# Performance work log

Hardware: AMD Instinct MI355X
Metric: run time of the kernel (lower is better)

## Reference

```python
import jax, jax.numpy as jnp
import numpy as np

N_NODES = 100000
IN_CH = 128
HID_CH = 128
N_EDGES = 1600000


def setup_inputs() -> dict:
    key = jax.random.key(0)
    ks = jax.random.split(key, 8)
    x = jax.random.normal(ks[0], (N_NODES, IN_CH), dtype=jnp.float32)
    edge_index = jax.random.randint(ks[1], (2, N_EDGES), 0, N_NODES, dtype=jnp.int64)
    s1 = 1.0 / np.sqrt(IN_CH)
    s2 = 1.0 / np.sqrt(HID_CH)
    # SAGEConv layer 1: lin_l (aggregated neighbors, has bias), lin_r (root)
    Wl1 = jax.random.uniform(ks[2], (IN_CH, HID_CH), jnp.float32, -s1, s1)
    Wr1 = jax.random.uniform(ks[3], (IN_CH, HID_CH), jnp.float32, -s1, s1)
    b1 = jnp.zeros((HID_CH,), jnp.float32)
    # SAGEConv layer 2
    Wl2 = jax.random.uniform(ks[4], (HID_CH, HID_CH), jnp.float32, -s2, s2)
    Wr2 = jax.random.uniform(ks[5], (HID_CH, HID_CH), jnp.float32, -s2, s2)
    b2 = jnp.zeros((HID_CH,), jnp.float32)
    return {"x": x, "edge_index": edge_index,
            "Wl1": Wl1, "Wr1": Wr1, "b1": b1,
            "Wl2": Wl2, "Wr2": Wr2, "b2": b2}


def _sage_conv(x, src, dst, inv_deg, Wl, Wr, b):
    # mean aggregation of source-node features into destination nodes
    agg = jax.ops.segment_sum(x[src], dst, num_segments=N_NODES)  # [N, d]
    mean = agg * inv_deg[:, None]
    # out = lin_l(mean_neighbors) + lin_r(x)
    return mean @ Wl + x @ Wr + b


def reference(x, edge_index, Wl1, Wr1, b1, Wl2, Wr2, b2):
    src = edge_index[0]
    dst = edge_index[1]
    deg = jax.ops.segment_sum(jnp.ones_like(dst, dtype=jnp.float32), dst,
                              num_segments=N_NODES)
    inv_deg = 1.0 / jnp.maximum(deg, 1.0)
    h = jax.nn.relu(_sage_conv(x, src, dst, inv_deg, Wl1, Wr1, b1))
    # F.dropout(p=0.2, training=False) is identity in eval mode
    h = jax.nn.relu(_sage_conv(h, src, dst, inv_deg, Wl2, Wr2, b2))
    return h
```

## Files before the change

### kernel.cpp

```cpp
#include <hip/hip_runtime.h>

#define NN 100000
#define NE 1600000
#define CH 128

#define PART 512
#define NP 196
#define PCAP 8704
#define NB 391
#define SCAP 64
#define SLAB 1536

typedef __attribute__((ext_vector_type(8))) short bf16x8;
typedef __attribute__((ext_vector_type(4))) float f32x4;
typedef unsigned int uint;
typedef unsigned short ushort;

__device__ __forceinline__ ushort f2b(float f) {
    uint u = __builtin_bit_cast(uint, f);
    uint r = (u + 0x7fff + ((u >> 16) & 1)) >> 16;
    return (ushort)r;
}
__device__ __forceinline__ float blo(uint v) { return __builtin_bit_cast(float, v << 16); }
__device__ __forceinline__ float bhi(uint v) { return __builtin_bit_cast(float, v & 0xffff0000u); }

__device__ __forceinline__ void acc8(float* a, uint4 v) {
    a[0] += blo(v.x); a[1] += bhi(v.x);
    a[2] += blo(v.y); a[3] += bhi(v.y);
    a[4] += blo(v.z); a[5] += bhi(v.z);
    a[6] += blo(v.w); a[7] += bhi(v.w);
}


__global__ __launch_bounds__(1024) void k_bin(const int4* __restrict__ src4, const int4* __restrict__ dst4,
                                              uint* __restrict__ pcnt, uint* __restrict__ pairbuf) {
    __shared__ uint slots[NP * SCAP];
    __shared__ uint lcnt[NP];
    __shared__ uint lbase[NP];
    int tid = threadIdx.x;
    if (tid < NP) lcnt[tid] = 0;
    __syncthreads();
    int e4 = blockIdx.x * 1024 + tid;
    if (e4 < NE / 4) {
        int4 d4 = dst4[e4];
        int4 s4 = src4[e4];
        int dd[4] = {d4.x, d4.y, d4.z, d4.w};
        int ss[4] = {s4.x, s4.y, s4.z, s4.w};
        #pragma unroll
        for (int j = 0; j < 4; ++j) {
            int p = dd[j] >> 9;
            uint pair = ((uint)(dd[j] & 511) << 17) | (uint)ss[j];
            uint pos = atomicAdd(&lcnt[p], 1u);
            if (pos < SCAP) slots[p * SCAP + pos] = pair;
        }
    }
    __syncthreads();
    if (tid < NP) {
        uint c = lcnt[tid];
        c = c < SCAP ? c : SCAP;
        lcnt[tid] = c;
        lbase[tid] = atomicAdd(&pcnt[tid], c);
    }
    __syncthreads();
    for (int t = tid; t < NP * SCAP; t += 1024) {
        int p = t >> 6;
        uint s = (uint)(t & (SCAP - 1));
        if (s < lcnt[p]) {
            uint idx = lbase[p] + s;
            if (idx < PCAP) pairbuf[(size_t)p * PCAP + idx] = slots[t];
        }
    }
}


__global__ __launch_bounds__(512) void k_mid(const uint* __restrict__ pcnt, const uint* __restrict__ pairbuf,
                                             int* __restrict__ nbrG, uint* __restrict__ pack,
                                             const float* __restrict__ x, ushort* __restrict__ xb,
                                             const float* __restrict__ Wl1, const float* __restrict__ Wr1,
                                             const float* __restrict__ Wl2, const float* __restrict__ Wr2,
                                             ushort* __restrict__ BtK1, ushort* __restrict__ BtK2) {
    __shared__ uint pairs[PCAP];
    __shared__ uint cnt[PART];
    __shared__ uint rowptr[PART + 1];
    __shared__ uint wpart[8];
    int tid = threadIdx.x;
    int b = blockIdx.x;
    if (b >= NP) {
        int i = b - NP;
        if (i < 784) {
            int p = i / 196;
            int n = (i % 196) * 512 + tid;
            if (n >= NN) return;
            const float4* sp = (const float4*)(x + (size_t)n * 128 + p * 32);
            uint4 o[4];
            ushort* op = (ushort*)o;
            #pragma unroll
            for (int q = 0; q < 8; ++q) {
                float4 v = sp[q];
                op[q * 4 + 0] = f2b(v.x);
                op[q * 4 + 1] = f2b(v.y);
                op[q * 4 + 2] = f2b(v.z);
                op[q * 4 + 3] = f2b(v.w);
            }
            uint4* dp = (uint4*)(xb + ((size_t)p * NN + n) * 32);
            #pragma unroll
            for (int q = 0; q < 4; ++q) dp[q] = o[q];
        } else {
            int idx = (i - 784) * 512 + tid;
            int L = idx >> 15;
            int ii = idx & 32767;
            const float* Wl = L ? Wl2 : Wl1;
            const float* Wr = L ? Wr2 : Wr1;
            ushort* BtK = L ? BtK2 : BtK1;
            int c = ii & 31;
            int n = (ii >> 5) & 127;
            int kt = ii >> 12;
            int k = kt * 32 + c;
            float v = (k < 128) ? Wl[k * 128 + n] : Wr[(k - 128) * 128 + n];
            BtK[ii] = f2b(v);
        }
        return;
    }
    int p = b;
    uint tot = pcnt[p];
    tot = tot < PCAP ? tot : PCAP;
    for (uint i = tid; i < tot; i += 512) pairs[i] = pairbuf[(size_t)p * PCAP + i];
    cnt[tid] = 0;
    __syncthreads();
    for (uint i = tid; i < tot; i += 512) atomicAdd(&cnt[pairs[i] >> 17], 1u);
    __syncthreads();
    uint deg = cnt[tid];
    uint s = deg;
    #pragma unroll
    for (int off = 1; off < 64; off <<= 1) {
        uint t = __shfl_up(s, off, 64);
        if ((tid & 63) >= off) s += t;
    }
    if ((tid & 63) == 63) wpart[tid >> 6] = s;
    __syncthreads();
    uint base = 0;
    int w = tid >> 6;
    #pragma unroll
    for (int q = 0; q < 7; ++q) base += (q < w) ? wpart[q] : 0;
    rowptr[tid] = base + s - deg;
    if (tid == 511) rowptr[512] = base + s;
    cnt[tid] = 0;
    __syncthreads();
    for (uint i = tid; i < tot; i += 512) {
        uint u = pairs[i];
        uint dl = u >> 17;
        uint pos = rowptr[dl] + atomicAdd(&cnt[dl], 1u);
        nbrG[(size_t)p * PCAP + pos] = (int)(u & 0x1FFFFu);
    }
    {
        int n = p * PART + tid;
        if (n < NN) {
            uint d = rowptr[tid + 1] - rowptr[tid];
            pack[n] = ((uint)(p * PCAP) + rowptr[tid]) | (d << 21);
        }
    }
}


__global__ __launch_bounds__(256) void k_agg(const uint4* __restrict__ feat, const int* __restrict__ nbrG,
                                             const uint* __restrict__ pack, uint4* __restrict__ outb) {
    __shared__ int sl[SLAB];
    __shared__ int sh_s0, sh_cnt;
    int plane = blockIdx.x;
    int nb = blockIdx.y * 64;
    int tid = threadIdx.x;
    int n = nb + (tid >> 2);
    int h = tid & 3;
    if (tid == 0) {
        uint u0 = pack[nb];
        int last = nb + 63 < NN ? nb + 63 : NN - 1;
        uint u1 = pack[last];
        int s0 = (int)(u0 & 0x1FFFFFu);
        sh_s0 = s0;
        sh_cnt = (int)(u1 & 0x1FFFFFu) + (int)(u1 >> 21) - s0;
    }
    __syncthreads();
    int s0 = sh_s0, scnt = sh_cnt;
    bool staged = scnt <= SLAB;
    if (staged) {
        for (int i = tid; i < scnt; i += 256) sl[i] = nbrG[s0 + i];
    }
    __syncthreads();
    if (n >= NN) return;
    uint u = pack[n];
    int s = (int)(u & 0x1FFFFFu);
    int d = (int)(u >> 21);
    const char* fb = (const char*)feat + ((size_t)plane * NN) * 64;
    uint hoff = (uint)h * 16;
    float a[8] = {};
    if (staged) {
        const int* bp = sl + (s - s0);
        int i = 0;
        for (; i + 8 <= d; i += 8) {
            uint off[8];
            uint4 v[8];
            #pragma unroll
            for (int j = 0; j < 8; ++j) off[j] = ((uint)bp[i + j] << 6) | hoff;
            #pragma unroll
            for (int j = 0; j < 8; ++j) v[j] = *(const uint4*)(fb + off[j]);
            #pragma unroll
            for (int j = 0; j < 8; ++j) acc8(a, v[j]);
        }
        for (; i < d; ++i) acc8(a, *(const uint4*)(fb + (((uint)bp[i] << 6) | hoff)));
    } else {
        const int* bp = nbrG + s;
        int i = 0;
        for (; i + 4 <= d; i += 4) {
            uint o0 = ((uint)bp[i] << 6) | hoff;
            uint o1 = ((uint)bp[i + 1] << 6) | hoff;
            uint o2 = ((uint)bp[i + 2] << 6) | hoff;
            uint o3 = ((uint)bp[i + 3] << 6) | hoff;
            uint4 v0 = *(const uint4*)(fb + o0);
            uint4 v1 = *(const uint4*)(fb + o1);
            uint4 v2 = *(const uint4*)(fb + o2);
            uint4 v3 = *(const uint4*)(fb + o3);
            acc8(a, v0);
            acc8(a, v1);
            acc8(a, v2);
            acc8(a, v3);
        }
        for (; i < d; ++i) acc8(a, *(const uint4*)(fb + (((uint)bp[i] << 6) | hoff)));
    }
    float id = 1.0f / fmaxf((float)d, 1.0f);
    uint4 r;
    r.x = (uint)f2b(a[0] * id) | ((uint)f2b(a[1] * id) << 16);
    r.y = (uint)f2b(a[2] * id) | ((uint)f2b(a[3] * id) << 16);
    r.z = (uint)f2b(a[4] * id) | ((uint)f2b(a[5] * id) << 16);
    r.w = (uint)f2b(a[6] * id) | ((uint)f2b(a[7] * id) << 16);
    outb[((size_t)plane * NN + n) * 4 + h] = r;
}


template <bool WB16>
__global__ __launch_bounds__(256) void k_gemm(const ushort* __restrict__ Am, const ushort* Ax,
                                              const ushort* __restrict__ BtK, const float* __restrict__ bias,
                                              void* outp, int M) {
    __shared__ char smem[17408];
    int tid = threadIdx.x;
    int lane = tid & 63;
    int w = tid >> 6;
    int bm = blockIdx.x * 64 + w * 16;
    int l16 = lane & 15;
    int g = lane >> 4;
    int lk8 = g * 8;

    int row = bm + l16;
    row = row < M ? row : M - 1;

    int uu0 = tid * 2;
    uint sw = ((uint)(tid >> 1) & 7) << 4;
    uint d0 = ((uint)uu0 * 16) ^ sw;
    uint d1 = ((uint)(uu0 + 1) * 16) ^ sw;
    uint rsw = ((uint)(l16 & 7)) << 4;

    {
        const uint4* gsrc = (const uint4*)BtK + uu0;
        uint4 r0 = gsrc[0], r1 = gsrc[1];
        *(uint4*)(smem + d0) = r0;
        *(uint4*)(smem + d1) = r1;
    }
    const ushort* A0 = Am;
    bf16x8 afc = *(const bf16x8*)(A0 + ((size_t)0 * NN + row) * 32 + lk8);
    __syncthreads();

    f32x4 acc[8] = {};
    #pragma unroll
    for (int kt = 0; kt < 8; ++kt) {
        int cur = kt & 1;
        uint4 r0, r1;
        bf16x8 afn;
        if (kt < 7) {
            const uint4* gsrc = (const uint4*)(BtK + (size_t)(kt + 1) * 4096) + uu0;
            r0 = gsrc[0];
            r1 = gsrc[1];
            const ushort* An = ((kt + 1) < 4) ? Am : Ax;
            int pn = (kt + 1) & 3;
            afn = *(const bf16x8*)(An + ((size_t)pn * NN + row) * 32 + lk8);
        }
        const char* bb = smem + cur * 8192;
        #pragma unroll
        for (int nt = 0; nt < 8; ++nt) {
            uint off = (((uint)(nt * 16 + l16) * 64) + (uint)g * 16) ^ rsw;
            bf16x8 bfr = *(const bf16x8*)(bb + off);
            acc[nt] = __builtin_amdgcn_mfma_f32_16x16x32_bf16(afc, bfr, acc[nt], 0, 0, 0);
        }
        if (kt < 7) {
            char* nb = smem + (cur ^ 1) * 8192;
            *(uint4*)(nb + d0) = r0;
            *(uint4*)(nb + d1) = r1;
            afc = afn;
        }
        __syncthreads();
    }

    int mr0 = g * 4;
    if (WB16) {
        ushort (*so)[136] = (ushort(*)[136])(smem + w * 4352);
        #pragma unroll
        for (int r = 0; r < 4; ++r)
            #pragma unroll
            for (int nt = 0; nt < 8; ++nt) {
                float v = acc[nt][r] + bias[nt * 16 + l16];
                so[mr0 + r][nt * 16 + l16] = f2b(v > 0.f ? v : 0.f);
            }
        #pragma unroll
        for (int pass = 0; pass < 4; ++pass) {
            int u = pass * 64 + lane;
            int rr = u >> 4, h16 = u & 15;
            int m = blockIdx.x * 64 + w * 16 + rr;
            if (m < M) {
                bf16x8 vv = *(const bf16x8*)&so[rr][h16 * 8];
                *(bf16x8*)((ushort*)outp + ((size_t)(h16 >> 2) * NN + m) * 32 + (h16 & 3) * 8) = vv;
            }
        }
    } else {
        #pragma unroll
        for (int r = 0; r < 4; ++r) {
            int m = bm + mr0 + r;
            if (m < M) {
                #pragma unroll
                for (int nt = 0; nt < 8; ++nt) {
                    float v = acc[nt][r] + bias[nt * 16 + l16];
                    ((float*)outp)[(size_t)m * 128 + nt * 16 + l16] = v > 0.f ? v : 0.f;
                }
            }
        }
    }
}


static inline size_t alignup(size_t x) { return (x + 255) & ~(size_t)255; }

extern "C" void kernel_launch(void* const* d_in, const int* in_sizes, int n_in,
                              void* d_out, int out_size, void* d_ws, size_t ws_size,
                              hipStream_t stream) {
    const float* x   = (const float*)d_in[0];
    const int* edge  = (const int*)d_in[1];
    const float* Wl1 = (const float*)d_in[2];
    const float* Wr1 = (const float*)d_in[3];
    const float* b1  = (const float*)d_in[4];
    const float* Wl2 = (const float*)d_in[5];
    const float* Wr2 = (const float*)d_in[6];
    const float* b2  = (const float*)d_in[7];
    float* out = (float*)d_out;

    const int* srcp = edge;
    const int* dstp = edge + NE;

    uint* pairbuf = (uint*)d_out;
    int* nbrG = (int*)d_out + (size_t)NP * PCAP;

    char* w = (char*)d_ws;
    uint* pcnt = (uint*)w;     w += alignup((size_t)NP * 4);
    uint* pack = (uint*)w;     w += alignup((size_t)NN * 4);
    ushort* xb = (ushort*)w;   w += alignup((size_t)NN * CH * 2);
    ushort* mb = (ushort*)w;   w += alignup((size_t)NN * CH * 2);
    ushort* BtK1 = (ushort*)w; w += alignup((size_t)128 * 256 * 2);
    ushort* BtK2 = (ushort*)w; w += alignup((size_t)128 * 256 * 2);

    hipMemsetAsync(pcnt, 0, (size_t)NP * 4, stream);

    k_bin<<<NB, 1024, 0, stream>>>((const int4*)srcp, (const int4*)dstp, pcnt, pairbuf);
    k_mid<<<NP + 784 + 128, 512, 0, stream>>>(pcnt, pairbuf, nbrG, pack,
                                              x, xb, Wl1, Wr1, Wl2, Wr2, BtK1, BtK2);

    int gg = (NN + 63) / 64;
    dim3 ag(4, (NN + 63) / 64);
    k_agg<<<ag, 256, 0, stream>>>((const uint4*)xb, nbrG, pack, (uint4*)mb);
    k_gemm<true><<<gg, 256, 0, stream>>>(mb, xb, BtK1, b1, (void*)xb, NN);
    k_agg<<<ag, 256, 0, stream>>>((const uint4*)xb, nbrG, pack, (uint4*)mb);
    k_gemm<false><<<gg, 256, 0, stream>>>(mb, xb, BtK2, b2, (void*)out, NN);
}
```

Measured before the change: 296.0 us.

## Replace two-level binning with global atomic count, scan, and scatter CSR build

Builds the CSR neighbor list by counting per-node degrees with global atomics, doing a per-partition block scan, and scattering source indices with global fill atomics. This replaces the shared-memory binning into partition buffers and the per-partition local sort. The aim is to cut the intermediate pairbuf round-trip and the LDS-heavy binning work. In exchange it relies on many contended global atomics with random-address scatter writes, adds a kernel launch, and leaves neighbor order within a row nondeterministic.

```diff
diff --git a/kernel.cpp b/kernel.cpp
--- a/kernel.cpp
+++ b/kernel.cpp
@@ -7,8 +7,6 @@
 #define PART 512
 #define NP 196
 #define PCAP 8704
-#define NB 391
-#define SCAP 64
 #define SLAB 1536
 
 typedef __attribute__((ext_vector_type(8))) short bf16x8;
@@ -32,104 +30,68 @@
 }
 
 
-__global__ __launch_bounds__(1024) void k_bin(const int4* __restrict__ src4, const int4* __restrict__ dst4,
-                                              uint* __restrict__ pcnt, uint* __restrict__ pairbuf) {
-    __shared__ uint slots[NP * SCAP];
-    __shared__ uint lcnt[NP];
-    __shared__ uint lbase[NP];
-    int tid = threadIdx.x;
-    if (tid < NP) lcnt[tid] = 0;
-    __syncthreads();
-    int e4 = blockIdx.x * 1024 + tid;
-    if (e4 < NE / 4) {
-        int4 d4 = dst4[e4];
-        int4 s4 = src4[e4];
-        int dd[4] = {d4.x, d4.y, d4.z, d4.w};
-        int ss[4] = {s4.x, s4.y, s4.z, s4.w};
-        #pragma unroll
-        for (int j = 0; j < 4; ++j) {
-            int p = dd[j] >> 9;
-            uint pair = ((uint)(dd[j] & 511) << 17) | (uint)ss[j];
-            uint pos = atomicAdd(&lcnt[p], 1u);
-            if (pos < SCAP) slots[p * SCAP + pos] = pair;
-        }
-    }
-    __syncthreads();
-    if (tid < NP) {
-        uint c = lcnt[tid];
-        c = c < SCAP ? c : SCAP;
-        lcnt[tid] = c;
-        lbase[tid] = atomicAdd(&pcnt[tid], c);
-    }
-    __syncthreads();
-    for (int t = tid; t < NP * SCAP; t += 1024) {
-        int p = t >> 6;
-        uint s = (uint)(t & (SCAP - 1));
-        if (s < lcnt[p]) {
-            uint idx = lbase[p] + s;
-            if (idx < PCAP) pairbuf[(size_t)p * PCAP + idx] = slots[t];
-        }
-    }
-}
-
-
-__global__ __launch_bounds__(512) void k_mid(const uint* __restrict__ pcnt, const uint* __restrict__ pairbuf,
-                                             int* __restrict__ nbrG, uint* __restrict__ pack,
+__global__ __launch_bounds__(512) void k_pre(const int4* __restrict__ dst4,
+                                             uint* __restrict__ cnt,
                                              const float* __restrict__ x, ushort* __restrict__ xb,
                                              const float* __restrict__ Wl1, const float* __restrict__ Wr1,
                                              const float* __restrict__ Wl2, const float* __restrict__ Wr2,
                                              ushort* __restrict__ BtK1, ushort* __restrict__ BtK2) {
-    __shared__ uint pairs[PCAP];
-    __shared__ uint cnt[PART];
-    __shared__ uint rowptr[PART + 1];
+    int tid = threadIdx.x;
+    int b = blockIdx.x;
+    if (b < 782) {
+        int e4 = b * 512 + tid;
+        if (e4 < NE / 4) {
+            int4 d4 = dst4[e4];
+            atomicAdd(&cnt[d4.x], 1u);
+            atomicAdd(&cnt[d4.y], 1u);
+            atomicAdd(&cnt[d4.z], 1u);
+            atomicAdd(&cnt[d4.w], 1u);
+        }
+        return;
+    }
+    int i = b - 782;
+    if (i < 784) {
+        int p = i / 196;
+        int n = (i % 196) * 512 + tid;
+        if (n >= NN) return;
+        const float4* sp = (const float4*)(x + (size_t)n * 128 + p * 32);
+        uint4 o[4];
+        ushort* op = (ushort*)o;
+        #pragma unroll
+        for (int q = 0; q < 8; ++q) {
+            float4 v = sp[q];
+            op[q * 4 + 0] = f2b(v.x);
+            op[q * 4 + 1] = f2b(v.y);
+            op[q * 4 + 2] = f2b(v.z);
+            op[q * 4 + 3] = f2b(v.w);
+        }
+        uint4* dp = (uint4*)(xb + ((size_t)p * NN + n) * 32);
+        #pragma unroll
+        for (int q = 0; q < 4; ++q) dp[q] = o[q];
+    } else {
+        int idx = (i - 784) * 512 + tid;
+        int L = idx >> 15;
+        int ii = idx & 32767;
+        const float* Wl = L ? Wl2 : Wl1;
+        const float* Wr = L ? Wr2 : Wr1;
+        ushort* BtK = L ? BtK2 : BtK1;
+        int c = ii & 31;
+        int n = (ii >> 5) & 127;
+        int kt = ii >> 12;
+        int k = kt * 32 + c;
+        float v = (k < 128) ? Wl[k * 128 + n] : Wr[(k - 128) * 128 + n];
+        BtK[ii] = f2b(v);
+    }
+}
+
+
+__global__ __launch_bounds__(512) void k_scan(const uint* __restrict__ cnt,
+                                              uint* __restrict__ pack, uint* __restrict__ fill) {
     __shared__ uint wpart[8];
     int tid = threadIdx.x;
-    int b = blockIdx.x;
-    if (b >= NP) {
-        int i = b - NP;
-        if (i < 784) {
-            int p = i / 196;
-            int n = (i % 196) * 512 + tid;
-            if (n >= NN) return;
-            const float4* sp = (const float4*)(x + (size_t)n * 128 + p * 32);
-            uint4 o[4];
-            ushort* op = (ushort*)o;
-            #pragma unroll
-            for (int q = 0; q < 8; ++q) {
-                float4 v = sp[q];
-                op[q * 4 + 0] = f2b(v.x);
-                op[q * 4 + 1] = f2b(v.y);
-                op[q * 4 + 2] = f2b(v.z);
-                op[q * 4 + 3] = f2b(v.w);
-            }
-            uint4* dp = (uint4*)(xb + ((size_t)p * NN + n) * 32);
-            #pragma unroll
-            for (int q = 0; q < 4; ++q) dp[q] = o[q];
-        } else {
-            int idx = (i - 784) * 512 + tid;
-            int L = idx >> 15;
-            int ii = idx & 32767;
-            const float* Wl = L ? Wl2 : Wl1;
-            const float* Wr = L ? Wr2 : Wr1;
-            ushort* BtK = L ? BtK2 : BtK1;
-            int c = ii & 31;
-            int n = (ii >> 5) & 127;
-            int kt = ii >> 12;
-            int k = kt * 32 + c;
-            float v = (k < 128) ? Wl[k * 128 + n] : Wr[(k - 128) * 128 + n];
-            BtK[ii] = f2b(v);
-        }
-        return;
-    }
-    int p = b;
-    uint tot = pcnt[p];
-    tot = tot < PCAP ? tot : PCAP;
-    for (uint i = tid; i < tot; i += 512) pairs[i] = pairbuf[(size_t)p * PCAP + i];
-    cnt[tid] = 0;
-    __syncthreads();
-    for (uint i = tid; i < tot; i += 512) atomicAdd(&cnt[pairs[i] >> 17], 1u);
-    __syncthreads();
-    uint deg = cnt[tid];
+    int p = blockIdx.x;
+    int n = p * PART + tid;
+    uint deg = (n < NN) ? cnt[n] : 0u;
     uint s = deg;
     #pragma unroll
     for (int off = 1; off < 64; off <<= 1) {
@@ -142,23 +104,28 @@
     int w = tid >> 6;
     #pragma unroll
     for (int q = 0; q < 7; ++q) base += (q < w) ? wpart[q] : 0;
-    rowptr[tid] = base + s - deg;
-    if (tid == 511) rowptr[512] = base + s;
-    cnt[tid] = 0;
-    __syncthreads();
-    for (uint i = tid; i < tot; i += 512) {
-        uint u = pairs[i];
-        uint dl = u >> 17;
-        uint pos = rowptr[dl] + atomicAdd(&cnt[dl], 1u);
-        nbrG[(size_t)p * PCAP + pos] = (int)(u & 0x1FFFFu);
-    }
-    {
-        int n = p * PART + tid;
-        if (n < NN) {
-            uint d = rowptr[tid + 1] - rowptr[tid];
-            pack[n] = ((uint)(p * PCAP) + rowptr[tid]) | (d << 21);
-        }
-    }
+    uint start = (uint)(p * PCAP) + base + s - deg;
+    if (n < NN) {
+        pack[n] = start | (deg << 21);
+        fill[n] = start;
+    }
+}
+
+
+__global__ __launch_bounds__(512) void k_scat(const int4* __restrict__ src4, const int4* __restrict__ dst4,
+                                              uint* __restrict__ fill, int* __restrict__ nbrG) {
+    int e4 = blockIdx.x * 512 + threadIdx.x;
+    if (e4 >= NE / 4) return;
+    int4 d4 = dst4[e4];
+    int4 s4 = src4[e4];
+    uint p0 = atomicAdd(&fill[d4.x], 1u);
+    uint p1 = atomicAdd(&fill[d4.y], 1u);
+    uint p2 = atomicAdd(&fill[d4.z], 1u);
+    uint p3 = atomicAdd(&fill[d4.w], 1u);
+    nbrG[p0] = s4.x;
+    nbrG[p1] = s4.y;
+    nbrG[p2] = s4.z;
+    nbrG[p3] = s4.w;
 }
 
 
@@ -352,22 +319,23 @@
     const int* srcp = edge;
     const int* dstp = edge + NE;
 
-    uint* pairbuf = (uint*)d_out;
-    int* nbrG = (int*)d_out + (size_t)NP * PCAP;
+    int* nbrG = (int*)d_out;
 
     char* w = (char*)d_ws;
-    uint* pcnt = (uint*)w;     w += alignup((size_t)NP * 4);
+    uint* cnt  = (uint*)w;     w += alignup((size_t)NN * 4);
+    uint* fill = (uint*)w;     w += alignup((size_t)NN * 4);
     uint* pack = (uint*)w;     w += alignup((size_t)NN * 4);
     ushort* xb = (ushort*)w;   w += alignup((size_t)NN * CH * 2);
     ushort* mb = (ushort*)w;   w += alignup((size_t)NN * CH * 2);
     ushort* BtK1 = (ushort*)w; w += alignup((size_t)128 * 256 * 2);
     ushort* BtK2 = (ushort*)w; w += alignup((size_t)128 * 256 * 2);
 
-    hipMemsetAsync(pcnt, 0, (size_t)NP * 4, stream);
-
-    k_bin<<<NB, 1024, 0, stream>>>((const int4*)srcp, (const int4*)dstp, pcnt, pairbuf);
-    k_mid<<<NP + 784 + 128, 512, 0, stream>>>(pcnt, pairbuf, nbrG, pack,
-                                              x, xb, Wl1, Wr1, Wl2, Wr2, BtK1, BtK2);
+    hipMemsetAsync(cnt, 0, (size_t)NN * 4, stream);
+
+    k_pre<<<782 + 784 + 128, 512, 0, stream>>>((const int4*)dstp, cnt,
+                                               x, xb, Wl1, Wr1, Wl2, Wr2, BtK1, BtK2);
+    k_scan<<<NP, 512, 0, stream>>>(cnt, pack, fill);
+    k_scat<<<782, 512, 0, stream>>>((const int4*)srcp, (const int4*)dstp, fill, nbrG);
 
     int gg = (NN + 63) / 64;
     dim3 ag(4, (NN + 63) / 64);
```

Measured after the change: 465.0 us. 1.57x slower.
